# Optimization experiments

Hardware: AMD Instinct MI355X
Metric: run time of the kernel (lower is better)

The kernel has to match this reference:

```python
import math
import jax, jax.numpy as jnp
from jax import lax
import numpy as np

NHEADS = 8
GN_GROUPS = 32
GN_EPS = 1e-5
L2_EPS = 1e-12


def conv2d(x, w, b=None, groups=1):
    # x: [B,C,H,W], w: [O, I/groups, kh, kw], stride 1, torch padding=k//2 (SAME)
    out = lax.conv_general_dilated(
        x, w, window_strides=(1, 1), padding='SAME',
        dimension_numbers=('NCHW', 'OIHW', 'NCHW'),
        feature_group_count=groups)
    if b is not None:
        out = out + b[None, :, None, None]
    return out


def group_norm(x, scale, bias, groups, eps=GN_EPS):
    B, C, H, W = x.shape
    xg = x.reshape(B, groups, C // groups, H, W)
    mu = jnp.mean(xg, axis=(2, 3, 4), keepdims=True)
    var = jnp.var(xg, axis=(2, 3, 4), keepdims=True)
    xg = (xg - mu) * lax.rsqrt(var + eps)
    x = xg.reshape(B, C, H, W)
    return x * scale[None, :, None, None] + bias[None, :, None, None]


def l2norm_ch(x):
    # F.normalize(x, dim=1): divide by channel L2 norm, clamped at eps
    n = jnp.sqrt(jnp.sum(x * x, axis=1, keepdims=True))
    return x / jnp.maximum(n, L2_EPS)


def attn_op(q, k, v, nheads, scale):
    # q,k,v: [B, C, xf, yf] real; tokens = frequency bins, features = C/nheads
    b, c, xf, yf = q.shape
    hd = c // nheads
    qh = q.reshape(b, nheads, hd, xf * yf)
    kh = k.reshape(b, nheads, hd, xf * yf)
    vh = v.reshape(b, nheads, hd, xf * yf)
    sim = jnp.einsum('bhcm,bhcn->bhmn', qh, kh) * scale
    attn = jax.nn.softmax(sim, axis=-1)
    out = jnp.einsum('bhmn,bhcn->bhcm', attn, vh)
    return out.reshape(b, c, xf, yf)


def setup_inputs() -> dict:
    key = jax.random.key(0)
    ks = jax.random.split(key, 14)
    B, H, W = 4, 48, 48
    fea = cond_c = qkv = dout = 256

    def rn(k, shape, s=0.05):
        return jax.random.normal(k, shape, dtype=jnp.float32) * s

    return {
        'x': jax.random.normal(ks[0], (B, fea, H, W), jnp.float32),
        'cond': jax.random.normal(ks[1], (B, cond_c, H, W), jnp.float32),
        'gn_w': jnp.ones((fea,), jnp.float32),
        'gn_b': jnp.zeros((fea,), jnp.float32),
        'q_dw': rn(ks[2], (fea, 1, 3, 3)),          # depthwise 3x3, groups=fea
        'q_pw_w': rn(ks[3], (qkv, fea, 1, 1)),
        'q_pw_b': jnp.zeros((qkv,), jnp.float32),
        'kv_dw': rn(ks[4], (cond_c, 1, 3, 3)),
        'kv_pw_w': rn(ks[5], (2 * qkv, cond_c, 1, 1)),
        'kv_pw_b': jnp.zeros((2 * qkv,), jnp.float32),
        'attn_out_w': rn(ks[6], (dout, qkv, 1, 1)),
        'attn_out_b': jnp.zeros((dout,), jnp.float32),
        'ffn_w1': rn(ks[7], (2 * dout, dout, 3, 3)),
        'ffn_w2': rn(ks[8], (dout, 2 * dout, 3, 3)),
        'ffn_w3': rn(ks[9], (dout, dout, 1, 1)),
        'ffn_b3': jnp.zeros((dout,), jnp.float32),
    }


def reference(x, cond, gn_w, gn_b, q_dw, q_pw_w, q_pw_b, kv_dw, kv_pw_w, kv_pw_b,
              attn_out_w, attn_out_b, ffn_w1, ffn_w2, ffn_w3, ffn_b3):
    B, C, H, W = x.shape
    qkv_dim = q_pw_w.shape[0]
    scale = 1.0 / math.sqrt(qkv_dim // NHEADS)

    xn = group_norm(x, gn_w, gn_b, GN_GROUPS)
    q = conv2d(conv2d(xn, q_dw, groups=C), q_pw_w, q_pw_b)
    kv = conv2d(conv2d(cond, kv_dw, groups=cond.shape[1]), kv_pw_w, kv_pw_b)
    k, v = jnp.split(kv, 2, axis=1)
    q, k, v = l2norm_ch(q), l2norm_ch(k), l2norm_ch(v)

    qf = jnp.fft.rfft2(q, axes=(-2, -1), norm='ortho')
    kf = jnp.fft.rfft2(k, axes=(-2, -1), norm='ortho')
    vf = jnp.fft.rfft2(v, axes=(-2, -1), norm='ortho')

    amp = attn_op(jnp.abs(qf), jnp.abs(kf), jnp.abs(vf), NHEADS, scale)
    phas = attn_op(jnp.angle(qf), jnp.angle(kf), jnp.angle(vf), NHEADS, scale)
    outc = lax.complex(amp * jnp.cos(phas), amp * jnp.sin(phas))  # torch.polar
    out = jnp.fft.irfft2(outc, s=(H, W), axes=(-2, -1), norm='ortho')

    attn_out = conv2d(out, attn_out_w, attn_out_b) + xn  # attn_res = Identity (fea_dim == dim_out)
    h1 = jax.nn.silu(conv2d(attn_out, ffn_w1))
    h2 = conv2d(h1, ffn_w2)
    ffn = conv2d(h2, ffn_w3, ffn_b3)
    # DropPath is identity in eval mode
    return ffn + attn_out
```

## Files before the change

kernel.cpp:

```cpp
#include <hip/hip_runtime.h>
#include <hip/hip_bf16.h>
#include <math.h>

constexpr int Bn = 4, Cn = 256, Hn = 48, Wn = 48, HW = 2304;
constexpr float ATT_SCALE = 0.17677669529663687f;

typedef __attribute__((ext_vector_type(8))) short bf16x8;
typedef __attribute__((ext_vector_type(4))) float f32x4;

#define MFMA16(A, B, C) __builtin_amdgcn_mfma_f32_16x16x32_bf16(A, B, C, 0, 0, 0)

__global__ void gn1_kernel(const float* __restrict__ x, float* __restrict__ part) {
  int bg = blockIdx.x >> 2, ck = blockIdx.x & 3;
  const float4* xp = (const float4*)(x + (size_t)bg * 18432 + ck * 4608);
  float s = 0.f, ss = 0.f;
  for (int i = threadIdx.x; i < 1152; i += 256) {
    float4 v = xp[i];
    s += v.x + v.y + v.z + v.w;
    ss += v.x * v.x + v.y * v.y + v.z * v.z + v.w * v.w;
  }
#pragma unroll
  for (int off = 32; off; off >>= 1) { s += __shfl_xor(s, off); ss += __shfl_xor(ss, off); }
  __shared__ float rs[4], rss[4];
  int wid = threadIdx.x >> 6;
  if ((threadIdx.x & 63) == 0) { rs[wid] = s; rss[wid] = ss; }
  __syncthreads();
  if (threadIdx.x == 0) {
    part[blockIdx.x * 2] = rs[0] + rs[1] + rs[2] + rs[3];
    part[blockIdx.x * 2 + 1] = rss[0] + rss[1] + rss[2] + rss[3];
  }
}

__global__ void gn2_kernel(const float* __restrict__ x, const float* __restrict__ part,
                           const float* __restrict__ gw, const float* __restrict__ gb,
                           float* __restrict__ y) {
  int bg = blockIdx.x >> 2, ck = blockIdx.x & 3;
  float s = part[bg * 8] + part[bg * 8 + 2] + part[bg * 8 + 4] + part[bg * 8 + 6];
  float ss = part[bg * 8 + 1] + part[bg * 8 + 3] + part[bg * 8 + 5] + part[bg * 8 + 7];
  float mean = s * (1.f / 18432.f);
  float var = ss * (1.f / 18432.f) - mean * mean;
  float inv = rsqrtf(var + 1e-5f);
  int g = bg & 31;
  const float4* xp = (const float4*)(x + (size_t)bg * 18432 + ck * 4608);
  float4* yp = (float4*)(y + (size_t)bg * 18432 + ck * 4608);
  for (int i = threadIdx.x; i < 1152; i += 256) {
    int c = (g << 3) + ((ck * 1152 + i) / 576);
    float w = gw[c] * inv, b = gb[c];
    float4 v = xp[i];
    v.x = (v.x - mean) * w + b; v.y = (v.y - mean) * w + b;
    v.z = (v.z - mean) * w + b; v.w = (v.w - mean) * w + b;
    yp[i] = v;
  }
}

__global__ void dw3x3_kernel(const float* __restrict__ in, const float* __restrict__ wd,
                             __hip_bfloat16* __restrict__ oh, __hip_bfloat16* __restrict__ ol) {
  int bc = blockIdx.x;
  int c = bc & 255;
  const float* ip = in + (size_t)bc * HW;
  const size_t ob = ((size_t)((bc >> 8) * 8 + (c >> 5)) * HW) * 32 + (c & 31);
  float w[9];
#pragma unroll
  for (int k = 0; k < 9; ++k) w[k] = wd[c * 9 + k];
  for (int p = threadIdx.x; p < HW; p += 256) {
    int yy = p / 48, xx = p - yy * 48;
    float a = 0.f;
#pragma unroll
    for (int ky = 0; ky < 3; ++ky) {
      int y2 = yy + ky - 1;
      if ((unsigned)y2 < 48u) {
#pragma unroll
        for (int kx = 0; kx < 3; ++kx) {
          int x2 = xx + kx - 1;
          if ((unsigned)x2 < 48u) a += ip[y2 * 48 + x2] * w[ky * 3 + kx];
        }
      }
    }
    __hip_bfloat16 h = __float2bfloat16(a);
    oh[ob + (size_t)p * 32] = h;
    ol[ob + (size_t)p * 32] = __float2bfloat16(a - __bfloat162float(h));
  }
}

__global__ void pwpack_kernel(const float* __restrict__ w, __hip_bfloat16* __restrict__ WH,
                              __hip_bfloat16* __restrict__ WL, int O) {
  int q = blockIdx.x * 256 + threadIdx.x;
  int o = q >> 8, c = q & 255;
  float v = w[q];
  __hip_bfloat16 h = __float2bfloat16(v);
  size_t idx = ((size_t)(c >> 5) * O + o) * 32 + (c & 31);
  WH[idx] = h;
  WL[idx] = __float2bfloat16(v - __bfloat162float(h));
}

template <bool RES>
__global__ void __launch_bounds__(256)
pw5_kernel(const __hip_bfloat16* __restrict__ XH, const __hip_bfloat16* __restrict__ XL,
           const __hip_bfloat16* __restrict__ WH, const __hip_bfloat16* __restrict__ WL,
           const float* __restrict__ bias, const float* __restrict__ res, size_t res_bs,
           float* __restrict__ out, size_t out_bs, int CO) {
  const int tid = threadIdx.x;
  const int wv = tid >> 6, lane = tid & 63, lm = lane & 15, kg = lane >> 4;
  const int px0 = blockIdx.x * 128;
  const int ob = blockIdx.y * 64;
  const int img = blockIdx.z;

  f32x4 acc[4][2];
#pragma unroll
  for (int mt = 0; mt < 4; ++mt) {
    acc[mt][0] = (f32x4){0.f, 0.f, 0.f, 0.f};
    acc[mt][1] = (f32x4){0.f, 0.f, 0.f, 0.f};
  }

  const size_t bb = (size_t)img * 589824 + (size_t)(px0 + wv * 32 + lm) * 32 + kg * 8;
#pragma unroll
  for (int ci = 0; ci < 8; ++ci) {
    const size_t bo = bb + (size_t)ci * 73728;
    bf16x8 BH0 = *(const bf16x8*)(XH + bo);
    bf16x8 BH1 = *(const bf16x8*)(XH + bo + 512);
    bf16x8 BL0 = *(const bf16x8*)(XL + bo);
    bf16x8 BL1 = *(const bf16x8*)(XL + bo + 512);
    const size_t wb = ((size_t)ci * CO + ob + lm) * 32 + kg * 8;
#pragma unroll
    for (int mt = 0; mt < 4; ++mt) {
      bf16x8 AH = *(const bf16x8*)(WH + wb + mt * 512);
      bf16x8 AL = *(const bf16x8*)(WL + wb + mt * 512);
      acc[mt][0] = MFMA16(AH, BH0, acc[mt][0]);
      acc[mt][0] = MFMA16(AH, BL0, acc[mt][0]);
      acc[mt][0] = MFMA16(AL, BH0, acc[mt][0]);
      acc[mt][1] = MFMA16(AH, BH1, acc[mt][1]);
      acc[mt][1] = MFMA16(AH, BL1, acc[mt][1]);
      acc[mt][1] = MFMA16(AL, BH1, acc[mt][1]);
    }
  }

#pragma unroll
  for (int mt = 0; mt < 4; ++mt) {
#pragma unroll
    for (int g = 0; g < 2; ++g) {
      int px = px0 + wv * 32 + g * 16 + lm;
#pragma unroll
      for (int r = 0; r < 4; ++r) {
        int o = ob + mt * 16 + kg * 4 + r;
        float v = acc[mt][g][r] + bias[o];
        if (RES) v += res[(size_t)img * res_bs + (size_t)o * HW + px];
        out[(size_t)img * out_bs + (size_t)o * HW + px] = v;
      }
    }
  }
}

__global__ void l2n_kernel(float* __restrict__ t, size_t bstride) {
  int pxl = threadIdx.x & 63;
  int cg = threadIdx.x >> 6;
  int p = blockIdx.x * 64 + pxl;
  float* q = t + (size_t)blockIdx.y * bstride + p;
  float ss = 0.f;
#pragma unroll 8
  for (int c = cg * 64; c < cg * 64 + 64; ++c) { float v = q[(size_t)c * HW]; ss += v * v; }
  __shared__ float part[4][64];
  __shared__ float sinv[64];
  part[cg][pxl] = ss;
  __syncthreads();
  if (threadIdx.x < 64) {
    float tot = part[0][pxl] + part[1][pxl] + part[2][pxl] + part[3][pxl];
    sinv[pxl] = 1.f / fmaxf(sqrtf(tot), 1e-12f);
  }
  __syncthreads();
  float inv = sinv[pxl];
#pragma unroll 8
  for (int c = cg * 64; c < cg * 64 + 64; ++c) q[(size_t)c * HW] *= inv;
}

__global__ void dftmat_kernel(__hip_bfloat16* __restrict__ mt) {
  int t = blockIdx.x * 256 + threadIdx.x;
  const float TP = 6.283185307179586f;
  if (t < 4096) {
    int up = t >> 6, w = t & 63;
    float v = 0.f;
    if (w < 48 && up < 50) {
      int u = (up < 25) ? up : up - 25;
      float ang = TP * (float)((w * u) % 48) / 48.f;
      v = ((up < 25) ? cosf(ang) : -sinf(ang)) * (1.f / 48.f);
    }
    __hip_bfloat16 h = __float2bfloat16(v);
    mt[t] = h; mt[4096 + t] = __float2bfloat16(v - __bfloat162float(h));
  } else if (t < 7168) {
    int q = t - 4096;
    int vv = q >> 6, h = q & 63;
    float c = 0.f, s = 0.f;
    if (h < 48) {
      float ang = TP * (float)((vv * h) % 48) / 48.f;
      c = cosf(ang); s = sinf(ang);
    }
    __hip_bfloat16 ch = __float2bfloat16(c);
    mt[8192 + q] = ch; mt[11264 + q] = __float2bfloat16(c - __bfloat162float(ch));
    __hip_bfloat16 sh = __float2bfloat16(s);
    mt[14336 + q] = sh; mt[17408 + q] = __float2bfloat16(s - __bfloat162float(sh));
  } else if (t < 8704) {
    int q = t - 7168;
    int w = q >> 5, u = q & 31;
    float c = 0.f, s = 0.f;
    if (u < 25) {
      float ang = TP * (float)((u * w) % 48) / 48.f;
      c = cosf(ang); s = -sinf(ang);
    }
    __hip_bfloat16 ch = __float2bfloat16(c);
    mt[20480 + q] = ch; mt[22016 + q] = __float2bfloat16(c - __bfloat162float(ch));
    __hip_bfloat16 sh = __float2bfloat16(s);
    mt[23552 + q] = sh; mt[25088 + q] = __float2bfloat16(s - __bfloat162float(sh));
  }
}

template <bool TLAY>
__global__ void __launch_bounds__(256)
rfft2_mfma(const float* __restrict__ in, size_t bstride, const __hip_bfloat16* __restrict__ mt,
           __hip_bfloat16* __restrict__ amp, __hip_bfloat16* __restrict__ pha) {
  const int bc = blockIdx.x;
  const int bi = bc >> 8, ch = bc & 255;
  const float* ip = in + (size_t)bi * bstride + (size_t)ch * HW;
  __shared__ __align__(16) __hip_bfloat16 XH[48 * 72], XL[48 * 72];
  __shared__ __align__(16) __hip_bfloat16 Yt[4][32 * 72];
  const int tid = threadIdx.x;
  const int lane = tid & 63, lm = lane & 15, kg = lane >> 4, wv = tid >> 6;

  for (int i = tid; i < 48 * 72; i += 256) {
    int r = i / 72, w = i - r * 72;
    float v = (w < 48) ? ip[r * 48 + w] : 0.f;
    __hip_bfloat16 h = __float2bfloat16(v);
    XH[i] = h;
    XL[i] = __float2bfloat16(v - __bfloat162float(h));
  }
  for (int i = tid; i < 4 * 32 * 72; i += 256) ((unsigned short*)Yt)[i] = 0;
  __syncthreads();

  {
    const __hip_bfloat16* W1TH = mt;
    const __hip_bfloat16* W1TL = mt + 4096;
    const int brow = wv * 16 + lm;
    bf16x8 BH0 = *(const bf16x8*)(W1TH + brow * 64 + kg * 8);
    bf16x8 BH1 = *(const bf16x8*)(W1TH + brow * 64 + 32 + kg * 8);
    bf16x8 BL0 = *(const bf16x8*)(W1TL + brow * 64 + kg * 8);
    bf16x8 BL1 = *(const bf16x8*)(W1TL + brow * 64 + 32 + kg * 8);
#pragma unroll
    for (int mtI = 0; mtI < 3; ++mtI) {
      f32x4 acc = {0.f, 0.f, 0.f, 0.f};
      bf16x8 AH = *(const bf16x8*)(&XH[(mtI * 16 + lm) * 72 + kg * 8]);
      bf16x8 AL = *(const bf16x8*)(&XL[(mtI * 16 + lm) * 72 + kg * 8]);
      acc = MFMA16(AH, BH0, acc); acc = MFMA16(AH, BL0, acc); acc = MFMA16(AL, BH0, acc);
      AH = *(const bf16x8*)(&XH[(mtI * 16 + lm) * 72 + 32 + kg * 8]);
      AL = *(const bf16x8*)(&XL[(mtI * 16 + lm) * 72 + 32 + kg * 8]);
      acc = MFMA16(AH, BH1, acc); acc = MFMA16(AH, BL1, acc); acc = MFMA16(AL, BH1, acc);
      if (brow < 50) {
        int aidx = (brow < 25) ? 0 : 2;
        int u = (brow < 25) ? brow : brow - 25;
#pragma unroll
        for (int r = 0; r < 4; ++r) {
          int h = mtI * 16 + kg * 4 + r;
          float v = acc[r];
          __hip_bfloat16 hh = __float2bfloat16(v);
          Yt[aidx][u * 72 + h] = hh;
          Yt[aidx + 1][u * 72 + h] = __float2bfloat16(v - __bfloat162float(hh));
        }
      }
    }
  }
  __syncthreads();

  {
    const __hip_bfloat16* M2CH = mt + 8192;
    const __hip_bfloat16* M2CL = mt + 11264;
    const __hip_bfloat16* M2SH = mt + 14336;
    const __hip_bfloat16* M2SL = mt + 17408;
    for (int t = wv; t < 6; t += 4) {
      int mtI = t >> 1, ntI = t & 1;
      f32x4 aC1 = {0.f,0.f,0.f,0.f}, aS1 = {0.f,0.f,0.f,0.f};
      f32x4 aC2 = {0.f,0.f,0.f,0.f}, aS2 = {0.f,0.f,0.f,0.f};
#pragma unroll
      for (int ks = 0; ks < 2; ++ks) {
        int arow = mtI * 16 + lm;
        int k0 = ks * 32 + kg * 8;
        bf16x8 CH = *(const bf16x8*)(M2CH + arow * 64 + k0);
        bf16x8 CL = *(const bf16x8*)(M2CL + arow * 64 + k0);
        bf16x8 SH = *(const bf16x8*)(M2SH + arow * 64 + k0);
        bf16x8 SL = *(const bf16x8*)(M2SL + arow * 64 + k0);
        int brow = ntI * 16 + lm;
        bf16x8 ReH = *(const bf16x8*)(&Yt[0][brow * 72 + k0]);
        bf16x8 ReL = *(const bf16x8*)(&Yt[1][brow * 72 + k0]);
        bf16x8 ImH = *(const bf16x8*)(&Yt[2][brow * 72 + k0]);
        bf16x8 ImL = *(const bf16x8*)(&Yt[3][brow * 72 + k0]);
        aC1 = MFMA16(CH, ReH, aC1); aC1 = MFMA16(CH, ReL, aC1); aC1 = MFMA16(CL, ReH, aC1);
        aS2 = MFMA16(SH, ImH, aS2); aS2 = MFMA16(SH, ImL, aS2); aS2 = MFMA16(SL, ImH, aS2);
        aC2 = MFMA16(CH, ImH, aC2); aC2 = MFMA16(CH, ImL, aC2); aC2 = MFMA16(CL, ImH, aC2);
        aS1 = MFMA16(SH, ReH, aS1); aS1 = MFMA16(SH, ReL, aS1); aS1 = MFMA16(SL, ReH, aS1);
      }
      int u = ntI * 16 + lm;
      if (u < 25) {
#pragma unroll
        for (int r = 0; r < 4; ++r) {
          int v = mtI * 16 + kg * 4 + r;
          float zre = aC1[r] + aS2[r];
          float zim = aC2[r] - aS1[r];
          float am = sqrtf(zre * zre + zim * zim);
          float ph = atan2f(zim, zre);
          int i = v * 25 + u;
          size_t o;
          if (TLAY) o = ((size_t)(bc >> 5) * 1200 + i) * 32 + (bc & 31);
          else      o = (size_t)bc * 1200 + i;
          amp[o] = __float2bfloat16(am);
          pha[o] = __float2bfloat16(ph);
        }
      }
    }
  }
}

__global__ void __launch_bounds__(256)
polar_irfft2_mfma(const float* __restrict__ amp, const float* __restrict__ pha,
                  const __hip_bfloat16* __restrict__ mt,
                  __hip_bfloat16* __restrict__ oh, __hip_bfloat16* __restrict__ ol) {
  const int bc = blockIdx.x;
  __shared__ __align__(16) __hip_bfloat16 Zt[4][32 * 72];
  __shared__ __align__(16) __hip_bfloat16 Yp[4][48 * 56];
  const int tid = threadIdx.x;
  const int lane = tid & 63, lm = lane & 15, kg = lane >> 4, wv = tid >> 6;

  for (int i = tid; i < 4 * 32 * 72; i += 256) ((unsigned short*)Zt)[i] = 0;
  for (int i = tid; i < 4 * 48 * 56; i += 256) ((unsigned short*)Yp)[i] = 0;
  __syncthreads();
  for (int i = tid; i < 1200; i += 256) {
    int v = i / 25, u = i - v * 25;
    float a = amp[(size_t)bc * 1200 + i];
    float p = pha[(size_t)bc * 1200 + i];
    float sc = (u == 0 || u == 24) ? (1.f / 48.f) : (2.f / 48.f);
    float zre = a * cosf(p) * sc;
    float zim = a * sinf(p) * sc;
    __hip_bfloat16 h0 = __float2bfloat16(zre);
    Zt[0][u * 72 + v] = h0;
    Zt[1][u * 72 + v] = __float2bfloat16(zre - __bfloat162float(h0));
    __hip_bfloat16 h1 = __float2bfloat16(zim);
    Zt[2][u * 72 + v] = h1;
    Zt[3][u * 72 + v] = __float2bfloat16(zim - __bfloat162float(h1));
  }
  __syncthreads();

  {
    const __hip_bfloat16* M2CH = mt + 8192;
    const __hip_bfloat16* M2CL = mt + 11264;
    const __hip_bfloat16* M2SH = mt + 14336;
    const __hip_bfloat16* M2SL = mt + 17408;
    for (int t = wv; t < 6; t += 4) {
      int mtI = t >> 1, ntI = t & 1;
      f32x4 aC1 = {0.f,0.f,0.f,0.f}, aS1 = {0.f,0.f,0.f,0.f};
      f32x4 aC2 = {0.f,0.f,0.f,0.f}, aS2 = {0.f,0.f,0.f,0.f};
#pragma unroll
      for (int ks = 0; ks < 2; ++ks) {
        int arow = mtI * 16 + lm;
        int k0 = ks * 32 + kg * 8;
        bf16x8 CH = *(const bf16x8*)(M2CH + arow * 64 + k0);
        bf16x8 CL = *(const bf16x8*)(M2CL + arow * 64 + k0);
        bf16x8 SH = *(const bf16x8*)(M2SH + arow * 64 + k0);
        bf16x8 SL = *(const bf16x8*)(M2SL + arow * 64 + k0);
        int brow = ntI * 16 + lm;
        bf16x8 ReH = *(const bf16x8*)(&Zt[0][brow * 72 + k0]);
        bf16x8 ReL = *(const bf16x8*)(&Zt[1][brow * 72 + k0]);
        bf16x8 ImH = *(const bf16x8*)(&Zt[2][brow * 72 + k0]);
        bf16x8 ImL = *(const bf16x8*)(&Zt[3][brow * 72 + k0]);
        aC1 = MFMA16(CH, ReH, aC1); aC1 = MFMA16(CH, ReL, aC1); aC1 = MFMA16(CL, ReH, aC1);
        aS2 = MFMA16(SH, ImH, aS2); aS2 = MFMA16(SH, ImL, aS2); aS2 = MFMA16(SL, ImH, aS2);
        aC2 = MFMA16(CH, ImH, aC2); aC2 = MFMA16(CH, ImL, aC2); aC2 = MFMA16(CL, ImH, aC2);
        aS1 = MFMA16(SH, ReH, aS1); aS1 = MFMA16(SH, ReL, aS1); aS1 = MFMA16(SL, ReH, aS1);
      }
      int u = ntI * 16 + lm;
      if (u < 25) {
#pragma unroll
        for (int r = 0; r < 4; ++r) {
          int h = mtI * 16 + kg * 4 + r;
          float yre = aC1[r] - aS2[r];
          float yim = aS1[r] + aC2[r];
          __hip_bfloat16 h0 = __float2bfloat16(yre);
          Yp[0][h * 56 + u] = h0;
          Yp[1][h * 56 + u] = __float2bfloat16(yre - __bfloat162float(h0));
          __hip_bfloat16 h1 = __float2bfloat16(yim);
          Yp[2][h * 56 + u] = h1;
          Yp[3][h * 56 + u] = __float2bfloat16(yim - __bfloat162float(h1));
        }
      }
    }
  }
  __syncthreads();

  {
    const __hip_bfloat16* W3CH = mt + 20480;
    const __hip_bfloat16* W3CL = mt + 22016;
    const __hip_bfloat16* W3SH = mt + 23552;
    const __hip_bfloat16* W3SL = mt + 25088;
    const int cch = bc & 255;
    const size_t obase = ((size_t)((bc >> 8) * 8 + (cch >> 5)) * HW) * 32 + (cch & 31);
    for (int t = wv; t < 9; t += 4) {
      int mtI = t / 3, ntI = t - (t / 3) * 3;
      f32x4 acc = {0.f, 0.f, 0.f, 0.f};
      int k0 = kg * 8;
      bf16x8 AH = *(const bf16x8*)(&Yp[0][(mtI * 16 + lm) * 56 + k0]);
      bf16x8 AL = *(const bf16x8*)(&Yp[1][(mtI * 16 + lm) * 56 + k0]);
      bf16x8 IH = *(const bf16x8*)(&Yp[2][(mtI * 16 + lm) * 56 + k0]);
      bf16x8 IL = *(const bf16x8*)(&Yp[3][(mtI * 16 + lm) * 56 + k0]);
      int brow = ntI * 16 + lm;
      bf16x8 CH = *(const bf16x8*)(W3CH + brow * 32 + k0);
      bf16x8 CL = *(const bf16x8*)(W3CL + brow * 32 + k0);
      bf16x8 SH = *(const bf16x8*)(W3SH + brow * 32 + k0);
      bf16x8 SL = *(const bf16x8*)(W3SL + brow * 32 + k0);
      acc = MFMA16(AH, CH, acc); acc = MFMA16(AH, CL, acc); acc = MFMA16(AL, CH, acc);
      acc = MFMA16(IH, SH, acc); acc = MFMA16(IH, SL, acc); acc = MFMA16(IL, SH, acc);
#pragma unroll
      for (int r = 0; r < 4; ++r) {
        int h = mtI * 16 + kg * 4 + r;
        int p = h * 48 + brow;
        float v = acc[r];
        __hip_bfloat16 hh = __float2bfloat16(v);
        oh[obase + (size_t)p * 32] = hh;
        ol[obase + (size_t)p * 32] = __float2bfloat16(v - __bfloat162float(hh));
      }
    }
  }
}

__global__ void __launch_bounds__(64)
attn_mfma5(const __hip_bfloat16* __restrict__ Qb, const __hip_bfloat16* __restrict__ Kb,
           const __hip_bfloat16* __restrict__ Vb, float* __restrict__ Ob) {
  const int lin = blockIdx.x;
  const int xcd = lin & 7;
  const int idx = lin >> 3;
  const int pr = xcd * 8 + idx / 75;
  const int m0 = (idx % 75) * 16;
  const int z = pr >> 5;
  const int bh = pr & 31;
  const __hip_bfloat16* Qt = Qb + (size_t)z * 1228800;
  const __hip_bfloat16* Kt = Kb + (size_t)z * 1228800;
  const __hip_bfloat16* Vc = Vb + (size_t)z * 1228800;
  float* Om = Ob + (size_t)z * 1228800;
  const int lane = threadIdx.x;
  const int lm = lane & 15, kg = lane >> 4;
  __shared__ unsigned short Pl[2][16][40];
  __shared__ float fl[16];
  __shared__ float linv[16];
  const __hip_bfloat16* Qp = Qt + ((size_t)bh * 1200 + m0) * 32;
  const __hip_bfloat16* Kp = Kt + (size_t)bh * 38400;
  const __hip_bfloat16* Vp = Vc + (size_t)bh * 38400;
  const bf16x8 qf = *(const bf16x8*)(Qp + lm * 32 + kg * 8);
  const float Cs = ATT_SCALE * 1.44269504f;

  f32x4 acc0 = {0.f, 0.f, 0.f, 0.f}, acc1 = {0.f, 0.f, 0.f, 0.f};
  float psum = 0.f, mreg = -3.0e38f;

  for (int G = 0; G < 19; ++G) {
    const int n0 = G * 64;
    const bool s3ok = (G < 18);
    bf16x8 kf0 = *(const bf16x8*)(Kp + (size_t)(n0 + lm) * 32 + kg * 8);
    bf16x8 kf1 = *(const bf16x8*)(Kp + (size_t)(n0 + 16 + lm) * 32 + kg * 8);
    bf16x8 kf2 = *(const bf16x8*)(Kp + (size_t)(n0 + 32 + lm) * 32 + kg * 8);
    __builtin_amdgcn_s_setprio(1);
    f32x4 d0 = {0.f, 0.f, 0.f, 0.f}; d0 = MFMA16(kf0, qf, d0);
    f32x4 d1 = {0.f, 0.f, 0.f, 0.f}; d1 = MFMA16(kf1, qf, d1);
    f32x4 d2 = {0.f, 0.f, 0.f, 0.f}; d2 = MFMA16(kf2, qf, d2);
    f32x4 d3 = {0.f, 0.f, 0.f, 0.f};
    if (s3ok) {
      bf16x8 kf3 = *(const bf16x8*)(Kp + (size_t)(n0 + 48 + lm) * 32 + kg * 8);
      d3 = MFMA16(kf3, qf, d3);
    }
    __builtin_amdgcn_s_setprio(0);
    float tm = fmaxf(fmaxf(fmaxf(d0[0], d0[1]), fmaxf(d0[2], d0[3])),
                     fmaxf(fmaxf(d1[0], d1[1]), fmaxf(d1[2], d1[3])));
    tm = fmaxf(tm, fmaxf(fmaxf(d2[0], d2[1]), fmaxf(d2[2], d2[3])));
    if (s3ok) tm = fmaxf(tm, fmaxf(fmaxf(d3[0], d3[1]), fmaxf(d3[2], d3[3])));
    tm = fmaxf(tm, __shfl_xor(tm, 16));
    tm = fmaxf(tm, __shfl_xor(tm, 32));
    const bool grow = (__ballot(tm > mreg) != 0ull);
    if (grow) {
      float nm = fmaxf(mreg, tm);
      float ff = exp2f((mreg - nm) * Cs);
      mreg = nm;
      if (kg == 0) fl[lm] = ff;
      psum *= ff;
    }
    const float mb = mreg * Cs;
    float p0 = exp2f(d0[0] * Cs - mb), p1 = exp2f(d0[1] * Cs - mb);
    float p2 = exp2f(d0[2] * Cs - mb), p3 = exp2f(d0[3] * Cs - mb);
    float p4 = exp2f(d1[0] * Cs - mb), p5 = exp2f(d1[1] * Cs - mb);
    float p6 = exp2f(d1[2] * Cs - mb), p7 = exp2f(d1[3] * Cs - mb);
    float p8 = exp2f(d2[0] * Cs - mb), p9 = exp2f(d2[1] * Cs - mb);
    float pa_ = exp2f(d2[2] * Cs - mb), pb_ = exp2f(d2[3] * Cs - mb);
    float ps = p0 + p1 + p2 + p3 + p4 + p5 + p6 + p7 + p8 + p9 + pa_ + pb_;
    ushort4 w0, w1, w2, w3;
    w0.x = __builtin_bit_cast(unsigned short, __float2bfloat16(p0));
    w0.y = __builtin_bit_cast(unsigned short, __float2bfloat16(p1));
    w0.z = __builtin_bit_cast(unsigned short, __float2bfloat16(p2));
    w0.w = __builtin_bit_cast(unsigned short, __float2bfloat16(p3));
    w1.x = __builtin_bit_cast(unsigned short, __float2bfloat16(p4));
    w1.y = __builtin_bit_cast(unsigned short, __float2bfloat16(p5));
    w1.z = __builtin_bit_cast(unsigned short, __float2bfloat16(p6));
    w1.w = __builtin_bit_cast(unsigned short, __float2bfloat16(p7));
    w2.x = __builtin_bit_cast(unsigned short, __float2bfloat16(p8));
    w2.y = __builtin_bit_cast(unsigned short, __float2bfloat16(p9));
    w2.z = __builtin_bit_cast(unsigned short, __float2bfloat16(pa_));
    w2.w = __builtin_bit_cast(unsigned short, __float2bfloat16(pb_));
    if (s3ok) {
      float pc_ = exp2f(d3[0] * Cs - mb), pd_ = exp2f(d3[1] * Cs - mb);
      float pe_ = exp2f(d3[2] * Cs - mb), pf_ = exp2f(d3[3] * Cs - mb);
      ps += pc_ + pd_ + pe_ + pf_;
      w3.x = __builtin_bit_cast(unsigned short, __float2bfloat16(pc_));
      w3.y = __builtin_bit_cast(unsigned short, __float2bfloat16(pd_));
      w3.z = __builtin_bit_cast(unsigned short, __float2bfloat16(pe_));
      w3.w = __builtin_bit_cast(unsigned short, __float2bfloat16(pf_));
    } else {
      w3.x = w3.y = w3.z = w3.w = 0;
    }
    psum += ps;
    *(ushort4*)(&Pl[0][lm][kg * 4]) = w0;
    *(ushort4*)(&Pl[0][lm][16 + kg * 4]) = w1;
    *(ushort4*)(&Pl[1][lm][kg * 4]) = w2;
    *(ushort4*)(&Pl[1][lm][16 + kg * 4]) = w3;
    if (grow) {
      float4 f4 = *(const float4*)(&fl[kg * 4]);
      acc0[0] *= f4.x; acc0[1] *= f4.y; acc0[2] *= f4.z; acc0[3] *= f4.w;
      acc1[0] *= f4.x; acc1[1] *= f4.y; acc1[2] *= f4.z; acc1[3] *= f4.w;
    }
    bf16x8 pa0 = *(const bf16x8*)(&Pl[0][lm][kg * 8]);
    bf16x8 pa1 = *(const bf16x8*)(&Pl[1][lm][kg * 8]);
    bf16x8 v00 = *(const bf16x8*)(Vp + (size_t)lm * 1200 + n0 + kg * 8);
    bf16x8 v01 = *(const bf16x8*)(Vp + (size_t)(16 + lm) * 1200 + n0 + kg * 8);
    bf16x8 v10 = *(const bf16x8*)(Vp + (size_t)lm * 1200 + n0 + 32 + kg * 8);
    bf16x8 v11 = *(const bf16x8*)(Vp + (size_t)(16 + lm) * 1200 + n0 + 32 + kg * 8);
    __builtin_amdgcn_s_setprio(1);
    acc0 = MFMA16(pa0, v00, acc0);
    acc1 = MFMA16(pa0, v01, acc1);
    acc0 = MFMA16(pa1, v10, acc0);
    acc1 = MFMA16(pa1, v11, acc1);
    __builtin_amdgcn_s_setprio(0);
  }
  psum += __shfl_xor(psum, 16);
  psum += __shfl_xor(psum, 32);
  if (kg == 0) linv[lm] = 1.f / psum;
  __syncthreads();
#pragma unroll
  for (int r = 0; r < 4; ++r) {
    int m = m0 + kg * 4 + r;
    float li = linv[kg * 4 + r];
    Om[(size_t)bh * 38400 + (size_t)lm * 1200 + m] = acc0[r] * li;
    Om[(size_t)bh * 38400 + (size_t)(16 + lm) * 1200 + m] = acc1[r] * li;
  }
}

template <int CIN>
__global__ void packw_kernel(const float* __restrict__ w, __hip_bfloat16* __restrict__ wp, int O) {
  int t = blockIdx.x * 256 + threadIdx.x;
  int o = t / CIN, c = t - o * CIN;
  if (o >= O) return;
  constexpr int NC = CIN / 32;
#pragma unroll
  for (int tap = 0; tap < 9; ++tap)
    wp[(((size_t)tap * NC + (c >> 5)) * O + o) * 32 + (c & 31)] = __float2bfloat16(w[(size_t)t * 9 + tap]);
}

__global__ void packx_kernel(const float* __restrict__ in, __hip_bfloat16* __restrict__ xp) {
  int y = blockIdx.x;
  int b = blockIdx.y;
  int c = threadIdx.x;
  const float* ip = in + ((size_t)(b * 256 + c) * 48 + y) * 48;
  __hip_bfloat16* op = xp + ((size_t)(b * 8 + (c >> 5)) * 2500 + (size_t)(y + 1) * 50 + 1) * 32 + (c & 31);
  for (int x = 0; x < 48; ++x) op[x * 32] = __float2bfloat16(ip[x]);
}

__global__ void addpack_kernel(const float* __restrict__ a, const float* __restrict__ b,
                               __hip_bfloat16* __restrict__ oh, __hip_bfloat16* __restrict__ ol) {
  int i = blockIdx.x * 256 + threadIdx.x;
  float4 x = ((const float4*)a)[i];
  float4 y = ((const float4*)b)[i];
  x.x += y.x; x.y += y.y; x.z += y.z; x.w += y.w;
  int e = i * 4;
  int img = e / 589824, rem = e - img * 589824;
  int c = rem / 2304, px = rem - c * 2304;
  size_t ob = ((size_t)(img * 8 + (c >> 5)) * HW) * 32 + (c & 31);
  float vv[4] = {x.x, x.y, x.z, x.w};
#pragma unroll
  for (int j = 0; j < 4; ++j) {
    __hip_bfloat16 h = __float2bfloat16(vv[j]);
    oh[ob + (size_t)(px + j) * 32] = h;
    ol[ob + (size_t)(px + j) * 32] = __float2bfloat16(vv[j] - __bfloat162float(h));
  }
}

template <int CIN, int CO, bool TO_PAD, int KS>
__global__ void __launch_bounds__(256)
mfconv3x3(const __hip_bfloat16* __restrict__ Xp, const __hip_bfloat16* __restrict__ Wp,
          __hip_bfloat16* __restrict__ Op, float* __restrict__ Of) {
  constexpr int NC = CIN / 32;
  constexpr int KC = NC / KS;
  constexpr int MT = CO / 32;
  const int q = gridDim.x >> 3;
  const int swz = (blockIdx.x & 7) * q + (blockIdx.x >> 3);
  const int mt = swz % MT;
  const int ks = (swz / MT) % KS;
  const int rq = swz / (MT * KS);
  const int img = rq / 12;
  const int y0b = (rq % 12) * 4;
  const int tid = threadIdx.x;
  const int wv = tid >> 6;
  const int y = y0b + wv;
  const int lane = tid & 63;
  const int lm = lane & 15, kg = lane >> 4;
  const int o0 = mt * 32;
  const int ci0 = ks * KC;

  __shared__ __hip_bfloat16 Als[9216];
  __shared__ __hip_bfloat16 Bls[9600];

  f32x4 acc[2][3];
#pragma unroll
  for (int f = 0; f < 2; ++f)
#pragma unroll
    for (int g = 0; g < 3; ++g) acc[f][g] = (f32x4){0.f, 0.f, 0.f, 0.f};

  for (int ci = 0; ci < KC; ++ci) {
    const int cic = ci0 + ci;
    const size_t wst = ((size_t)cic * CO + o0) * 32;
    const size_t bst = ((size_t)(img * NC + cic) * 2500 + (size_t)y0b * 50) * 32;
    __syncthreads();
    for (int c = tid; c < 2352; c += 256) {
      if (c < 1152) {
        int tap = c >> 7, rem = c & 127;
        float4 v = *(const float4*)(Wp + wst + (size_t)tap * (NC * CO * 32) + rem * 8);
        *(float4*)(&Als[c * 8]) = v;
      } else {
        int c2 = c - 1152;
        float4 v = *(const float4*)(Xp + bst + (size_t)c2 * 8);
        *(float4*)(&Bls[c2 * 8]) = v;
      }
    }
    __syncthreads();
#pragma unroll
    for (int tap = 0; tap < 9; ++tap) {
      const int dy = tap / 3 - 1, dx = tap - (tap / 3) * 3 - 1;
      bf16x8 A0 = *(const bf16x8*)(&Als[tap * 1024 + lm * 32 + kg * 8]);
      bf16x8 A1 = *(const bf16x8*)(&Als[tap * 1024 + 512 + lm * 32 + kg * 8]);
      const int bbase = ((wv + 1 + dy) * 50 + 1 + dx + lm) * 32 + kg * 8;
      bf16x8 B0 = *(const bf16x8*)(&Bls[bbase]);
      bf16x8 B1 = *(const bf16x8*)(&Bls[bbase + 512]);
      bf16x8 B2 = *(const bf16x8*)(&Bls[bbase + 1024]);
      acc[0][0] = MFMA16(A0, B0, acc[0][0]);
      acc[0][1] = MFMA16(A0, B1, acc[0][1]);
      acc[0][2] = MFMA16(A0, B2, acc[0][2]);
      acc[1][0] = MFMA16(A1, B0, acc[1][0]);
      acc[1][1] = MFMA16(A1, B1, acc[1][1]);
      acc[1][2] = MFMA16(A1, B2, acc[1][2]);
    }
  }

  if (TO_PAD) {
    const int cio = o0 >> 5;
#pragma unroll
    for (int f = 0; f < 2; ++f) {
      const int cc = f * 16 + kg * 4;
#pragma unroll
      for (int g = 0; g < 3; ++g) {
        int x = g * 16 + lm;
        ushort4 st;
        float v0 = acc[f][g][0], v1 = acc[f][g][1], v2 = acc[f][g][2], v3 = acc[f][g][3];
        v0 = v0 / (1.f + __expf(-v0)); v1 = v1 / (1.f + __expf(-v1));
        v2 = v2 / (1.f + __expf(-v2)); v3 = v3 / (1.f + __expf(-v3));
        st.x = __builtin_bit_cast(unsigned short, __float2bfloat16(v0));
        st.y = __builtin_bit_cast(unsigned short, __float2bfloat16(v1));
        st.z = __builtin_bit_cast(unsigned short, __float2bfloat16(v2));
        st.w = __builtin_bit_cast(unsigned short, __float2bfloat16(v3));
        *(ushort4*)(Op + (((size_t)(img * (CO / 32) + cio) * 2500 + (size_t)(y + 1) * 50 + (x + 1)) * 32 + cc)) = st;
      }
    }
  } else {
    float* Ofp = Of + (size_t)ks * 4 * CO * HW;
#pragma unroll
    for (int f = 0; f < 2; ++f)
#pragma unroll
      for (int g = 0; g < 3; ++g) {
        int x = g * 16 + lm;
#pragma unroll
        for (int r = 0; r < 4; ++r) {
          int o = o0 + f * 16 + kg * 4 + r;
          Ofp[((size_t)img * CO + o) * HW + y * 48 + x] = acc[f][g][r];
        }
      }
  }
}

extern "C" void kernel_launch(void* const* d_in, const int* in_sizes, int n_in,
                              void* d_out, int out_size, void* d_ws, size_t ws_size,
                              hipStream_t stream) {
  (void)in_sizes; (void)n_in; (void)out_size; (void)ws_size;
  const float* x      = (const float*)d_in[0];
  const float* cond   = (const float*)d_in[1];
  const float* gn_w   = (const float*)d_in[2];
  const float* gn_b   = (const float*)d_in[3];
  const float* q_dw   = (const float*)d_in[4];
  const float* q_pw_w = (const float*)d_in[5];
  const float* q_pw_b = (const float*)d_in[6];
  const float* kv_dw  = (const float*)d_in[7];
  const float* kv_pw_w= (const float*)d_in[8];
  const float* kv_pw_b= (const float*)d_in[9];
  const float* ao_w   = (const float*)d_in[10];
  const float* ao_b   = (const float*)d_in[11];
  const float* w1     = (const float*)d_in[12];
  const float* w2     = (const float*)d_in[13];
  const float* w3     = (const float*)d_in[14];
  const float* b3     = (const float*)d_in[15];
  float* ws = (float*)d_ws;
  float* Yo = (float*)d_out;

  const size_t U = 2359296;
  const size_t Hf = 1228800;
  const size_t CS = 589824;
  const size_t CS2 = 1179648;

  float* XN  = ws;
  __hip_bfloat16* DWH = (__hip_bfloat16*)(ws + U);
  __hip_bfloat16* DWL = DWH + 2359296;
  float* Qb  = ws + 2 * U;
  float* KV  = ws + 3 * U;
  __hip_bfloat16* AQT = (__hip_bfloat16*)(ws + 5 * U);
  __hip_bfloat16* PQT = AQT + 1228800;
  __hip_bfloat16* AKT = AQT + 2 * 1228800;
  __hip_bfloat16* PKT = AQT + 3 * 1228800;
  __hip_bfloat16* AVc = AQT + 4 * 1228800;
  __hip_bfloat16* PVc = AQT + 5 * 1228800;
  float* AO  = ws + 5 * U + 3 * Hf;
  float* PO  = AO + Hf;
  __hip_bfloat16* OUTH = (__hip_bfloat16*)(ws + U);
  __hip_bfloat16* OUTL = OUTH + 2359296;
  float* ATT = ws + 5 * U;
  __hip_bfloat16* Xp1 = (__hip_bfloat16*)(ws + U);
  __hip_bfloat16* Xp2 = (__hip_bfloat16*)(ws + 2 * U);
  __hip_bfloat16* Wp1 = (__hip_bfloat16*)(ws + 2 * U + 2600000);
  __hip_bfloat16* Wp2 = (__hip_bfloat16*)(ws + 2 * U + 3200000);
  float* H2  = ws;
  float* H2b = ws + U;
  __hip_bfloat16* H2H = (__hip_bfloat16*)(ws + 5 * U + 3 * Hf);
  __hip_bfloat16* H2L = H2H + 2359296;
  __hip_bfloat16* BW = (__hip_bfloat16*)(ws + 5 * U + 5 * Hf);
  __hip_bfloat16* QWH = BW,            * QWL = BW + 65536;
  __hip_bfloat16* KWH = BW + 131072,   * KWL = BW + 262144;
  __hip_bfloat16* AWH = BW + 393216,   * AWL = BW + 458752;
  __hip_bfloat16* W3H = BW + 524288,   * W3L = BW + 589824;
  __hip_bfloat16* MT  = BW + 655360;
  float* GNP = ws + 5 * U + 5 * Hf + 341000;

  pwpack_kernel<<<256, 256, 0, stream>>>(q_pw_w, QWH, QWL, 256);
  pwpack_kernel<<<512, 256, 0, stream>>>(kv_pw_w, KWH, KWL, 512);
  pwpack_kernel<<<256, 256, 0, stream>>>(ao_w, AWH, AWL, 256);
  pwpack_kernel<<<256, 256, 0, stream>>>(w3, W3H, W3L, 256);
  dftmat_kernel<<<34, 256, 0, stream>>>(MT);
  gn1_kernel<<<512, 256, 0, stream>>>(x, GNP);
  gn2_kernel<<<512, 256, 0, stream>>>(x, GNP, gn_w, gn_b, XN);
  dw3x3_kernel<<<1024, 256, 0, stream>>>(XN, q_dw, DWH, DWL);
  pw5_kernel<false><<<dim3(18, 4, 4), 256, 0, stream>>>(DWH, DWL, QWH, QWL, q_pw_b, nullptr, 0, Qb, CS, 256);
  dw3x3_kernel<<<1024, 256, 0, stream>>>(cond, kv_dw, DWH, DWL);
  pw5_kernel<false><<<dim3(18, 8, 4), 256, 0, stream>>>(DWH, DWL, KWH, KWL, kv_pw_b, nullptr, 0, KV, CS2, 512);
  l2n_kernel<<<dim3(36, 4), 256, 0, stream>>>(Qb, CS);
  l2n_kernel<<<dim3(36, 4), 256, 0, stream>>>(KV, CS2);
  l2n_kernel<<<dim3(36, 4), 256, 0, stream>>>(KV + CS, CS2);
  rfft2_mfma<true ><<<1024, 256, 0, stream>>>(Qb, CS, MT, AQT, PQT);
  rfft2_mfma<true ><<<1024, 256, 0, stream>>>(KV, CS2, MT, AKT, PKT);
  rfft2_mfma<false><<<1024, 256, 0, stream>>>(KV + CS, CS2, MT, AVc, PVc);
  attn_mfma5<<<4800, 64, 0, stream>>>(AQT, AKT, AVc, AO);
  polar_irfft2_mfma<<<1024, 256, 0, stream>>>(AO, PO, MT, OUTH, OUTL);
  pw5_kernel<true><<<dim3(18, 4, 4), 256, 0, stream>>>(OUTH, OUTL, AWH, AWL, ao_b, XN, CS, ATT, CS, 256);
  hipMemsetAsync(Xp1, 0, 2560000 * sizeof(__hip_bfloat16), stream);
  hipMemsetAsync(Xp2, 0, 5120000 * sizeof(__hip_bfloat16), stream);
  packx_kernel<<<dim3(48, 4), 256, 0, stream>>>(ATT, Xp1);
  packw_kernel<256><<<512, 256, 0, stream>>>(w1, Wp1, 512);
  packw_kernel<512><<<512, 256, 0, stream>>>(w2, Wp2, 256);
  mfconv3x3<256, 512, true, 1><<<768, 256, 0, stream>>>(Xp1, Wp1, Xp2, nullptr);
  mfconv3x3<512, 256, false, 2><<<768, 256, 0, stream>>>(Xp2, Wp2, nullptr, H2);
  addpack_kernel<<<2304, 256, 0, stream>>>(H2, H2b, H2H, H2L);
  pw5_kernel<true><<<dim3(18, 4, 4), 256, 0, stream>>>(H2H, H2L, W3H, W3L, b3, ATT, CS, Yo, CS, 256);
}
```

Measured before the change: 479.7 us.

## Merge small setup, l2norm, rfft and packing launches into combined kernels

```diff
diff --git a/kernel.cpp b/kernel.cpp
--- a/kernel.cpp
+++ b/kernel.cpp
@@ -82,15 +82,65 @@
   }
 }
 
-__global__ void pwpack_kernel(const float* __restrict__ w, __hip_bfloat16* __restrict__ WH,
-                              __hip_bfloat16* __restrict__ WL, int O) {
-  int q = blockIdx.x * 256 + threadIdx.x;
-  int o = q >> 8, c = q & 255;
-  float v = w[q];
-  __hip_bfloat16 h = __float2bfloat16(v);
-  size_t idx = ((size_t)(c >> 5) * O + o) * 32 + (c & 31);
-  WH[idx] = h;
-  WL[idx] = __float2bfloat16(v - __bfloat162float(h));
+__global__ void setup_kernel(const float* __restrict__ q_pw_w, const float* __restrict__ kv_pw_w,
+                             const float* __restrict__ ao_w, const float* __restrict__ w3,
+                             __hip_bfloat16* __restrict__ QWH, __hip_bfloat16* __restrict__ QWL,
+                             __hip_bfloat16* __restrict__ KWH, __hip_bfloat16* __restrict__ KWL,
+                             __hip_bfloat16* __restrict__ AWH, __hip_bfloat16* __restrict__ AWL,
+                             __hip_bfloat16* __restrict__ W3H, __hip_bfloat16* __restrict__ W3L,
+                             __hip_bfloat16* __restrict__ mt) {
+  const int b = blockIdx.x, tid = threadIdx.x;
+  if (b < 1280) {
+    const float* w; __hip_bfloat16 *WH, *WL; int O, q;
+    if (b < 256)       { w = q_pw_w;  WH = QWH; WL = QWL; O = 256; q = b * 256 + tid; }
+    else if (b < 768)  { w = kv_pw_w; WH = KWH; WL = KWL; O = 512; q = (b - 256) * 256 + tid; }
+    else if (b < 1024) { w = ao_w;    WH = AWH; WL = AWL; O = 256; q = (b - 768) * 256 + tid; }
+    else               { w = w3;      WH = W3H; WL = W3L; O = 256; q = (b - 1024) * 256 + tid; }
+    int o = q >> 8, c = q & 255;
+    float v = w[q];
+    __hip_bfloat16 h = __float2bfloat16(v);
+    size_t idx = ((size_t)(c >> 5) * O + o) * 32 + (c & 31);
+    WH[idx] = h;
+    WL[idx] = __float2bfloat16(v - __bfloat162float(h));
+  } else {
+    int t = (b - 1280) * 256 + tid;
+    const float TP = 6.283185307179586f;
+    if (t < 4096) {
+      int up = t >> 6, w = t & 63;
+      float v = 0.f;
+      if (w < 48 && up < 50) {
+        int u = (up < 25) ? up : up - 25;
+        float ang = TP * (float)((w * u) % 48) / 48.f;
+        v = ((up < 25) ? cosf(ang) : -sinf(ang)) * (1.f / 48.f);
+      }
+      __hip_bfloat16 h = __float2bfloat16(v);
+      mt[t] = h; mt[4096 + t] = __float2bfloat16(v - __bfloat162float(h));
+    } else if (t < 7168) {
+      int q = t - 4096;
+      int vv = q >> 6, h = q & 63;
+      float c = 0.f, s = 0.f;
+      if (h < 48) {
+        float ang = TP * (float)((vv * h) % 48) / 48.f;
+        c = cosf(ang); s = sinf(ang);
+      }
+      __hip_bfloat16 ch = __float2bfloat16(c);
+      mt[8192 + q] = ch; mt[11264 + q] = __float2bfloat16(c - __bfloat162float(ch));
+      __hip_bfloat16 sh = __float2bfloat16(s);
+      mt[14336 + q] = sh; mt[17408 + q] = __float2bfloat16(s - __bfloat162float(sh));
+    } else if (t < 8704) {
+      int q = t - 7168;
+      int w = q >> 5, u = q & 31;
+      float c = 0.f, s = 0.f;
+      if (u < 25) {
+        float ang = TP * (float)((u * w) % 48) / 48.f;
+        c = cosf(ang); s = -sinf(ang);
+      }
+      __hip_bfloat16 ch = __float2bfloat16(c);
+      mt[20480 + q] = ch; mt[22016 + q] = __float2bfloat16(c - __bfloat162float(ch));
+      __hip_bfloat16 sh = __float2bfloat16(s);
+      mt[23552 + q] = sh; mt[25088 + q] = __float2bfloat16(s - __bfloat162float(sh));
+    }
+  }
 }
 
 template <bool RES>
@@ -150,11 +200,15 @@
   }
 }
 
-__global__ void l2n_kernel(float* __restrict__ t, size_t bstride) {
+__global__ void l2n3_kernel(float* __restrict__ Qb, float* __restrict__ KV) {
+  int t = blockIdx.y >> 2;
+  int img = blockIdx.y & 3;
+  float* base = (t == 0) ? Qb : (t == 1 ? KV : KV + 589824);
+  size_t bstride = (t == 0) ? (size_t)589824 : (size_t)1179648;
   int pxl = threadIdx.x & 63;
   int cg = threadIdx.x >> 6;
   int p = blockIdx.x * 64 + pxl;
-  float* q = t + (size_t)blockIdx.y * bstride + p;
+  float* q = base + (size_t)img * bstride + p;
   float ss = 0.f;
 #pragma unroll 8
   for (int c = cg * 64; c < cg * 64 + 64; ++c) { float v = q[(size_t)c * HW]; ss += v * v; }
@@ -172,53 +226,18 @@
   for (int c = cg * 64; c < cg * 64 + 64; ++c) q[(size_t)c * HW] *= inv;
 }
 
-__global__ void dftmat_kernel(__hip_bfloat16* __restrict__ mt) {
-  int t = blockIdx.x * 256 + threadIdx.x;
-  const float TP = 6.283185307179586f;
-  if (t < 4096) {
-    int up = t >> 6, w = t & 63;
-    float v = 0.f;
-    if (w < 48 && up < 50) {
-      int u = (up < 25) ? up : up - 25;
-      float ang = TP * (float)((w * u) % 48) / 48.f;
-      v = ((up < 25) ? cosf(ang) : -sinf(ang)) * (1.f / 48.f);
-    }
-    __hip_bfloat16 h = __float2bfloat16(v);
-    mt[t] = h; mt[4096 + t] = __float2bfloat16(v - __bfloat162float(h));
-  } else if (t < 7168) {
-    int q = t - 4096;
-    int vv = q >> 6, h = q & 63;
-    float c = 0.f, s = 0.f;
-    if (h < 48) {
-      float ang = TP * (float)((vv * h) % 48) / 48.f;
-      c = cosf(ang); s = sinf(ang);
-    }
-    __hip_bfloat16 ch = __float2bfloat16(c);
-    mt[8192 + q] = ch; mt[11264 + q] = __float2bfloat16(c - __bfloat162float(ch));
-    __hip_bfloat16 sh = __float2bfloat16(s);
-    mt[14336 + q] = sh; mt[17408 + q] = __float2bfloat16(s - __bfloat162float(sh));
-  } else if (t < 8704) {
-    int q = t - 7168;
-    int w = q >> 5, u = q & 31;
-    float c = 0.f, s = 0.f;
-    if (u < 25) {
-      float ang = TP * (float)((u * w) % 48) / 48.f;
-      c = cosf(ang); s = -sinf(ang);
-    }
-    __hip_bfloat16 ch = __float2bfloat16(c);
-    mt[20480 + q] = ch; mt[22016 + q] = __float2bfloat16(c - __bfloat162float(ch));
-    __hip_bfloat16 sh = __float2bfloat16(s);
-    mt[23552 + q] = sh; mt[25088 + q] = __float2bfloat16(s - __bfloat162float(sh));
-  }
-}
-
-template <bool TLAY>
 __global__ void __launch_bounds__(256)
-rfft2_mfma(const float* __restrict__ in, size_t bstride, const __hip_bfloat16* __restrict__ mt,
-           __hip_bfloat16* __restrict__ amp, __hip_bfloat16* __restrict__ pha) {
-  const int bc = blockIdx.x;
+rfft2_all(const float* __restrict__ Qb, const float* __restrict__ KV,
+          const __hip_bfloat16* __restrict__ mt, __hip_bfloat16* __restrict__ spec) {
+  const int t = blockIdx.x >> 10;
+  const int bc = blockIdx.x & 1023;
   const int bi = bc >> 8, ch = bc & 255;
-  const float* ip = in + (size_t)bi * bstride + (size_t)ch * HW;
+  const float* src = (t == 0) ? Qb : (t == 1 ? KV : KV + 589824);
+  const size_t bstride = (t == 0) ? (size_t)589824 : (size_t)1179648;
+  const float* ip = src + (size_t)bi * bstride + (size_t)ch * HW;
+  __hip_bfloat16* amp = spec + (size_t)(2 * t) * 1228800;
+  __hip_bfloat16* pha = spec + (size_t)(2 * t + 1) * 1228800;
+  const bool tlay = (t < 2);
   __shared__ __align__(16) __hip_bfloat16 XH[48 * 72], XL[48 * 72];
   __shared__ __align__(16) __hip_bfloat16 Yt[4][32 * 72];
   const int tid = threadIdx.x;
@@ -272,8 +291,8 @@
     const __hip_bfloat16* M2CL = mt + 11264;
     const __hip_bfloat16* M2SH = mt + 14336;
     const __hip_bfloat16* M2SL = mt + 17408;
-    for (int t = wv; t < 6; t += 4) {
-      int mtI = t >> 1, ntI = t & 1;
+    for (int tt = wv; tt < 6; tt += 4) {
+      int mtI = tt >> 1, ntI = tt & 1;
       f32x4 aC1 = {0.f,0.f,0.f,0.f}, aS1 = {0.f,0.f,0.f,0.f};
       f32x4 aC2 = {0.f,0.f,0.f,0.f}, aS2 = {0.f,0.f,0.f,0.f};
 #pragma unroll
@@ -305,7 +324,7 @@
           float ph = atan2f(zim, zre);
           int i = v * 25 + u;
           size_t o;
-          if (TLAY) o = ((size_t)(bc >> 5) * 1200 + i) * 32 + (bc & 31);
+          if (tlay) o = ((size_t)(bc >> 5) * 1200 + i) * 32 + (bc & 31);
           else      o = (size_t)bc * 1200 + i;
           amp[o] = __float2bfloat16(am);
           pha[o] = __float2bfloat16(ph);
@@ -551,24 +570,47 @@
   }
 }
 
-template <int CIN>
-__global__ void packw_kernel(const float* __restrict__ w, __hip_bfloat16* __restrict__ wp, int O) {
-  int t = blockIdx.x * 256 + threadIdx.x;
-  int o = t / CIN, c = t - o * CIN;
-  if (o >= O) return;
-  constexpr int NC = CIN / 32;
-#pragma unroll
-  for (int tap = 0; tap < 9; ++tap)
-    wp[(((size_t)tap * NC + (c >> 5)) * O + o) * 32 + (c & 31)] = __float2bfloat16(w[(size_t)t * 9 + tap]);
-}
-
-__global__ void packx_kernel(const float* __restrict__ in, __hip_bfloat16* __restrict__ xp) {
-  int y = blockIdx.x;
-  int b = blockIdx.y;
-  int c = threadIdx.x;
-  const float* ip = in + ((size_t)(b * 256 + c) * 48 + y) * 48;
-  __hip_bfloat16* op = xp + ((size_t)(b * 8 + (c >> 5)) * 2500 + (size_t)(y + 1) * 50 + 1) * 32 + (c & 31);
-  for (int x = 0; x < 48; ++x) op[x * 32] = __float2bfloat16(ip[x]);
+__global__ void pack3_kernel(const float* __restrict__ w1, const float* __restrict__ w2,
+                             const float* __restrict__ att,
+                             __hip_bfloat16* __restrict__ Wp1, __hip_bfloat16* __restrict__ Wp2,
+                             __hip_bfloat16* __restrict__ xp, __hip_bfloat16* __restrict__ Xp2) {
+  const int b = blockIdx.x, tid = threadIdx.x;
+  if (b < 512) {
+    int t = b * 256 + tid;
+    int o = t >> 8, c = t & 255;
+#pragma unroll
+    for (int tap = 0; tap < 9; ++tap)
+      Wp1[(((size_t)tap * 8 + (c >> 5)) * 512 + o) * 32 + (c & 31)] = __float2bfloat16(w1[(size_t)t * 9 + tap]);
+  } else if (b < 1024) {
+    int t = (b - 512) * 256 + tid;
+    int o = t >> 9, c = t & 511;
+#pragma unroll
+    for (int tap = 0; tap < 9; ++tap)
+      Wp2[(((size_t)tap * 16 + (c >> 5)) * 256 + o) * 32 + (c & 31)] = __float2bfloat16(w2[(size_t)t * 9 + tap]);
+  } else if (b < 1216) {
+    int s = b - 1024;
+    int y = s % 48, img = s / 48;
+    int c = tid;
+    const float* ip = att + ((size_t)(img * 256 + c) * 48 + y) * 48;
+    __hip_bfloat16* op = xp + ((size_t)(img * 8 + (c >> 5)) * 2500 + (size_t)(y + 1) * 50 + 1) * 32 + (c & 31);
+    for (int x = 0; x < 48; ++x) op[x * 32] = __float2bfloat16(ip[x]);
+  } else {
+    int idx = (b - 1216) * 256 + tid;
+    if (idx < 18816) {
+      __hip_bfloat16* base;
+      int plane, cell;
+      if (idx < 6272) { base = xp; plane = idx / 196; cell = idx % 196; }
+      else { int j = idx - 6272; base = Xp2; plane = j / 196; cell = j % 196; }
+      int row, col;
+      if (cell < 50) { row = 0; col = cell; }
+      else if (cell < 100) { row = 49; col = cell - 50; }
+      else if (cell < 148) { row = 1 + (cell - 100); col = 0; }
+      else { row = 1 + (cell - 148); col = 49; }
+      float4* p = (float4*)(base + ((size_t)plane * 2500 + row * 50 + col) * 32);
+      float4 z = make_float4(0.f, 0.f, 0.f, 0.f);
+      p[0] = z; p[1] = z; p[2] = z; p[3] = z;
+    }
+  }
 }
 
 __global__ void addpack_kernel(const float* __restrict__ a, const float* __restrict__ b,
@@ -725,11 +767,8 @@
   float* Qb  = ws + 2 * U;
   float* KV  = ws + 3 * U;
   __hip_bfloat16* AQT = (__hip_bfloat16*)(ws + 5 * U);
-  __hip_bfloat16* PQT = AQT + 1228800;
   __hip_bfloat16* AKT = AQT + 2 * 1228800;
-  __hip_bfloat16* PKT = AQT + 3 * 1228800;
   __hip_bfloat16* AVc = AQT + 4 * 1228800;
-  __hip_bfloat16* PVc = AQT + 5 * 1228800;
   float* AO  = ws + 5 * U + 3 * Hf;
   float* PO  = AO + Hf;
   __hip_bfloat16* OUTH = (__hip_bfloat16*)(ws + U);
@@ -751,31 +790,20 @@
   __hip_bfloat16* MT  = BW + 655360;
   float* GNP = ws + 5 * U + 5 * Hf + 341000;
 
-  pwpack_kernel<<<256, 256, 0, stream>>>(q_pw_w, QWH, QWL, 256);
-  pwpack_kernel<<<512, 256, 0, stream>>>(kv_pw_w, KWH, KWL, 512);
-  pwpack_kernel<<<256, 256, 0, stream>>>(ao_w, AWH, AWL, 256);
-  pwpack_kernel<<<256, 256, 0, stream>>>(w3, W3H, W3L, 256);
-  dftmat_kernel<<<34, 256, 0, stream>>>(MT);
+  setup_kernel<<<1314, 256, 0, stream>>>(q_pw_w, kv_pw_w, ao_w, w3,
+                                         QWH, QWL, KWH, KWL, AWH, AWL, W3H, W3L, MT);
   gn1_kernel<<<512, 256, 0, stream>>>(x, GNP);
   gn2_kernel<<<512, 256, 0, stream>>>(x, GNP, gn_w, gn_b, XN);
   dw3x3_kernel<<<1024, 256, 0, stream>>>(XN, q_dw, DWH, DWL);
   pw5_kernel<false><<<dim3(18, 4, 4), 256, 0, stream>>>(DWH, DWL, QWH, QWL, q_pw_b, nullptr, 0, Qb, CS, 256);
   dw3x3_kernel<<<1024, 256, 0, stream>>>(cond, kv_dw, DWH, DWL);
   pw5_kernel<false><<<dim3(18, 8, 4), 256, 0, stream>>>(DWH, DWL, KWH, KWL, kv_pw_b, nullptr, 0, KV, CS2, 512);
-  l2n_kernel<<<dim3(36, 4), 256, 0, stream>>>(Qb, CS);
-  l2n_kernel<<<dim3(36, 4), 256, 0, stream>>>(KV, CS2);
-  l2n_kernel<<<dim3(36, 4), 256, 0, stream>>>(KV + CS, CS2);
-  rfft2_mfma<true ><<<1024, 256, 0, stream>>>(Qb, CS, MT, AQT, PQT);
-  rfft2_mfma<true ><<<1024, 256, 0, stream>>>(KV, CS2, MT, AKT, PKT);
-  rfft2_mfma<false><<<1024, 256, 0, stream>>>(KV + CS, CS2, MT, AVc, PVc);
+  l2n3_kernel<<<dim3(36, 12), 256, 0, stream>>>(Qb, KV);
+  rfft2_all<<<3072, 256, 0, stream>>>(Qb, KV, MT, AQT);
   attn_mfma5<<<4800, 64, 0, stream>>>(AQT, AKT, AVc, AO);
   polar_irfft2_mfma<<<1024, 256, 0, stream>>>(AO, PO, MT, OUTH, OUTL);
   pw5_kernel<true><<<dim3(18, 4, 4), 256, 0, stream>>>(OUTH, OUTL, AWH, AWL, ao_b, XN, CS, ATT, CS, 256);
-  hipMemsetAsync(Xp1, 0, 2560000 * sizeof(__hip_bfloat16), stream);
-  hipMemsetAsync(Xp2, 0, 5120000 * sizeof(__hip_bfloat16), stream);
-  packx_kernel<<<dim3(48, 4), 256, 0, stream>>>(ATT, Xp1);
-  packw_kernel<256><<<512, 256, 0, stream>>>(w1, Wp1, 512);
-  packw_kernel<512><<<512, 256, 0, stream>>>(w2, Wp2, 256);
+  pack3_kernel<<<1290, 256, 0, stream>>>(w1, w2, ATT, Wp1, Wp2, Xp1, Xp2);
   mfconv3x3<256, 512, true, 1><<<768, 256, 0, stream>>>(Xp1, Wp1, Xp2, nullptr);
   mfconv3x3<512, 256, false, 2><<<768, 256, 0, stream>>>(Xp2, Wp2, nullptr, H2);
   addpack_kernel<<<2304, 256, 0, stream>>>(H2, H2b, H2H, H2L);
```

After: 428.3 us. 1.12x faster.
